# Kernel tuning notes

Measured on AMD Instinct MI355X. Metric: run time of the kernel, lower is better.

The kernel has to match this reference:

```python
import jax, jax.numpy as jnp
import numpy as np

N_NODES = 100000
N_EDGES = 1600000
IN_F = 64
OUT_F = 32
NEG_SLOPE = 0.2


def setup_inputs() -> dict:
    key = jax.random.key(0)
    k = jax.random.split(key, 6)
    x = jax.random.normal(k[0], (N_NODES, IN_F), dtype=jnp.float32)
    edge_index = jax.random.randint(k[1], (2, N_EDGES), 0, N_NODES, dtype=jnp.int64)
    W = jax.random.normal(k[2], (IN_F, OUT_F), dtype=jnp.float32) * 0.1
    att_src = jax.random.normal(k[3], (OUT_F,), dtype=jnp.float32) * 0.1
    att_dst = jax.random.normal(k[4], (OUT_F,), dtype=jnp.float32) * 0.1
    bias = jax.random.normal(k[5], (OUT_F,), dtype=jnp.float32) * 0.1
    return {"x": x, "edge_index": edge_index, "W": W,
            "att_src": att_src, "att_dst": att_dst, "bias": bias}


def reference(x, edge_index, W, att_src, att_dst, bias):
    N = x.shape[0]
    # Linear projection (single head, concat=True -> [N, OUT_F])
    h = x @ W  # [N, C]
    a_src = h @ att_src  # [N] per-node source attention logit contribution
    a_dst = h @ att_dst  # [N] per-node destination contribution
    # add self loops (PyG GATConv default add_self_loops=True)
    loop = jnp.arange(N, dtype=edge_index.dtype)
    src = jnp.concatenate([edge_index[0], loop])  # [E+N] message senders
    dst = jnp.concatenate([edge_index[1], loop])  # [E+N] message receivers
    # attention logits per edge, LeakyReLU(alpha_src[j] + alpha_dst[i])
    e = jax.nn.leaky_relu(a_src[src] + a_dst[dst], NEG_SLOPE)
    # segment softmax over incoming edges of each destination node
    m = jax.ops.segment_max(e, dst, num_segments=N)  # every node has a self loop
    ex = jnp.exp(e - m[dst])
    denom = jax.ops.segment_sum(ex, dst, num_segments=N)
    alpha = ex / denom[dst]  # [E+N]
    # weighted scatter-add of source features into destinations
    out = jax.ops.segment_sum(h[src] * alpha[:, None], dst, num_segments=N)
    out = out + bias
    # GATLayer activation='relu'
    return jax.nn.relu(out)
```

## Files before the change

kernel.cpp:

```cpp
#include <hip/hip_runtime.h>
#include <hip/hip_fp16.h>
#include <math.h>

#define IN_F 64
#define OUT_F 32
#define NEG_SLOPE 0.2f

#define BK_SHIFT 7
#define BK 128
#define NBMAX 1024
#define NBLKA 256
#define PSTAGE 10

typedef _Float16 half8_t __attribute__((ext_vector_type(8)));
typedef float float4_t __attribute__((ext_vector_type(4)));

__device__ __forceinline__ float leaky(float v) {
    return (v > 0.0f) ? v : NEG_SLOPE * v;
}

__device__ __forceinline__ int incScan256(int v, int tid, int* wsum) {
    const int lane = tid & 63, wid = tid >> 6;
    #pragma unroll
    for (int m = 1; m < 64; m <<= 1) {
        int u = __shfl_up(v, m);
        if (lane >= m) v += u;
    }
    if (lane == 63) wsum[wid] = v;
    __syncthreads();
    int add = 0;
    for (int k = 0; k < wid; ++k) add += wsum[k];
    __syncthreads();
    return v + add;
}

__device__ __forceinline__ int incScan512(int v, int tid, int* wsum) {
    const int lane = tid & 63, wid = tid >> 6;
    #pragma unroll
    for (int m = 1; m < 64; m <<= 1) {
        int u = __shfl_up(v, m);
        if (lane >= m) v += u;
    }
    if (lane == 63) wsum[wid] = v;
    __syncthreads();
    int add = 0;
    for (int k = 0; k < wid; ++k) add += wsum[k];
    __syncthreads();
    return v + add;
}

__global__ __launch_bounds__(256) void k_projhist(
        const float* __restrict__ x, const float* __restrict__ W,
        const float* __restrict__ att_src, const float* __restrict__ att_dst,
        __half2* __restrict__ h2, float* __restrict__ asrc, float* __restrict__ adst,
        const int* __restrict__ dst, int* __restrict__ hist,
        int N, int NB, int E, int epb, int PB) {
    __shared__ int smem[2560];
    const int tid = threadIdx.x;

    if (blockIdx.x >= PB) {
        int* lh = smem;
        const int blk = blockIdx.x - PB;
        for (int i = tid; i < NB; i += 256) lh[i] = 0;
        __syncthreads();
        const int e0 = blk * epb, e1 = min(E, e0 + epb);
        for (int e = e0 + tid; e < e1; e += 256) atomicAdd(&lh[dst[e] >> BK_SHIFT], 1);
        __syncthreads();
        for (int b = tid; b < NB; b += 256) hist[(size_t)b * NBLKA + blk] = lh[b];
        return;
    }

    const int wv   = tid >> 6;
    const int lane = tid & 63;
    const int m    = lane & 15;
    const int quad = lane >> 4;
    const int node0 = (blockIdx.x * 4 + wv) * 16;
    if (node0 >= N) return;

    const int kb = quad * 8;
    half8_t b00, b01, b10, b11;
    #pragma unroll
    for (int j = 0; j < 8; ++j) {
        b00[j] = (_Float16)W[(kb + j) * OUT_F + m];
        b01[j] = (_Float16)W[(32 + kb + j) * OUT_F + m];
        b10[j] = (_Float16)W[(kb + j) * OUT_F + 16 + m];
        b11[j] = (_Float16)W[(32 + kb + j) * OUT_F + 16 + m];
    }
    const int row = min(node0 + m, N - 1);
    const float* xr = x + (size_t)row * IN_F + kb;
    float4_t xa = *(const float4_t*)(xr);
    float4_t xb = *(const float4_t*)(xr + 4);
    float4_t xc = *(const float4_t*)(xr + 32);
    float4_t xd = *(const float4_t*)(xr + 36);
    half8_t a0, a1;
    #pragma unroll
    for (int j = 0; j < 4; ++j) {
        a0[j] = (_Float16)xa[j]; a0[4 + j] = (_Float16)xb[j];
        a1[j] = (_Float16)xc[j]; a1[4 + j] = (_Float16)xd[j];
    }
    float4_t acc0 = {0.f, 0.f, 0.f, 0.f};
    float4_t acc1 = {0.f, 0.f, 0.f, 0.f};
    acc0 = __builtin_amdgcn_mfma_f32_16x16x32_f16(a0, b00, acc0, 0, 0, 0);
    acc0 = __builtin_amdgcn_mfma_f32_16x16x32_f16(a1, b01, acc0, 0, 0, 0);
    acc1 = __builtin_amdgcn_mfma_f32_16x16x32_f16(a0, b10, acc1, 0, 0, 0);
    acc1 = __builtin_amdgcn_mfma_f32_16x16x32_f16(a1, b11, acc1, 0, 0, 0);

    const float aS0 = att_src[m], aS1 = att_src[16 + m];
    const float aD0 = att_dst[m], aD1 = att_dst[16 + m];
    #pragma unroll
    for (int r = 0; r < 4; ++r) {
        const int node = node0 + quad * 4 + r;
        float h0 = acc0[r], h1 = acc1[r];
        float h0p = __shfl_xor(h0, 1);
        float h1p = __shfl_xor(h1, 1);
        if (node < N && (m & 1) == 0) {
            __half2 hv;
            hv.x = __float2half_rn(h0); hv.y = __float2half_rn(h0p);
            h2[(size_t)node * 16 + (m >> 1)] = hv;
            __half2 hw;
            hw.x = __float2half_rn(h1); hw.y = __float2half_rn(h1p);
            h2[(size_t)node * 16 + 8 + (m >> 1)] = hw;
        }
        float vs = h0 * aS0 + h1 * aS1;
        float vd = h0 * aD0 + h1 * aD1;
        #pragma unroll
        for (int mm = 1; mm < 16; mm <<= 1) {
            vs += __shfl_xor(vs, mm);
            vd += __shfl_xor(vd, mm);
        }
        if (node < N && m == 0) {
            asrc[node] = vs;
            adst[node] = vd;
        }
    }
}

__global__ __launch_bounds__(256) void k_scan1(int* __restrict__ hist,
                                               int* __restrict__ bsum, int NB) {
    __shared__ int wsum[4];
    const int b = blockIdx.x, tid = threadIdx.x;
    int v = hist[(size_t)b * NBLKA + tid];
    const int inc = incScan256(v, tid, wsum);
    hist[(size_t)b * NBLKA + tid] = inc - v;
    if (tid == 255) bsum[b] = inc;
}

__global__ __launch_bounds__(512) void k_bpart(const int* __restrict__ src,
                                               const int* __restrict__ dst,
                                               const int* __restrict__ hist,
                                               const int* __restrict__ bsum,
                                               int* __restrict__ recs,
                                               int NB, int E, int epb) {
    __shared__ int tt[NBMAX];
    __shared__ int lcur[NBMAX];
    __shared__ int wsum[8];
    const int tid = threadIdx.x, blk = blockIdx.x;
    for (int i = tid; i < NBMAX; i += 512) tt[i] = (i < NB) ? bsum[i] : 0;
    __syncthreads();
    {
        int a0 = tt[tid * 2], a1 = tt[tid * 2 + 1];
        int s = a0 + a1;
        int inc = incScan512(s, tid, wsum);
        int run = inc - s;
        tt[tid * 2] = run; run += a0;
        tt[tid * 2 + 1] = run;
    }
    __syncthreads();
    for (int b = tid; b < NB; b += 512)
        lcur[b] = hist[(size_t)b * NBLKA + blk] + tt[b];
    __syncthreads();
    const int e0 = blk * epb, e1 = min(E, e0 + epb);
    for (int e = e0 + tid; e < e1; e += 512) {
        int s = src[e];
        int d = dst[e];
        int p = atomicAdd(&lcur[d >> BK_SHIFT], 1);
        recs[p] = ((d & (BK - 1)) << 17) | s;
    }
}

__global__ __launch_bounds__(256) void k_place(const int* __restrict__ recs,
                                               const int* __restrict__ bsum,
                                               int* __restrict__ cnt,
                                               int* __restrict__ offs,
                                               int* __restrict__ col,
                                               int NB, int E, int N) {
    __shared__ int tt[NBMAX];
    __shared__ int fineCnt[BK];
    __shared__ int cur[BK];
    __shared__ int wsum[4];
    const int b = blockIdx.x, tid = threadIdx.x;
    for (int i = tid; i < NBMAX; i += 256) tt[i] = (i < NB) ? bsum[i] : 0;
    __syncthreads();
    {
        int a0 = tt[tid * 4], a1 = tt[tid * 4 + 1], a2 = tt[tid * 4 + 2], a3 = tt[tid * 4 + 3];
        int s = a0 + a1 + a2 + a3;
        int inc = incScan256(s, tid, wsum);
        int run = inc - s;
        tt[tid * 4] = run;     run += a0;
        tt[tid * 4 + 1] = run; run += a1;
        tt[tid * 4 + 2] = run; run += a2;
        tt[tid * 4 + 3] = run;
    }
    __syncthreads();
    const int cb0 = tt[b];
    const int cb1 = (b + 1 < NB) ? tt[b + 1] : E;
    const int count = cb1 - cb0;
    int myrec[PSTAGE];
    if (tid < BK) fineCnt[tid] = 0;
    __syncthreads();
    #pragma unroll
    for (int k = 0; k < PSTAGE; ++k) {
        int i = tid + k * 256;
        if (i < count) {
            int v = recs[cb0 + i];
            myrec[k] = v;
            atomicAdd(&fineCnt[v >> 17], 1);
        }
    }
    for (int i = tid + PSTAGE * 256; i < count; i += 256)
        atomicAdd(&fineCnt[recs[cb0 + i] >> 17], 1);
    __syncthreads();
    const int v0 = (tid < BK) ? fineCnt[tid] : 0;
    const int inc = incScan256(v0, tid, wsum);
    const int excl = inc - v0;
    if (tid < BK) {
        const int node = (b << BK_SHIFT) + tid;
        if (node < N) {
            cnt[node]  = v0;
            offs[node] = cb0 + excl;
        }
        cur[tid] = cb0 + excl;
    }
    __syncthreads();
    #pragma unroll
    for (int k = 0; k < PSTAGE; ++k) {
        int i = tid + k * 256;
        if (i < count) {
            int r = myrec[k];
            int p = atomicAdd(&cur[r >> 17], 1);
            col[p] = r & 0x1FFFF;
        }
    }
    for (int i = tid + PSTAGE * 256; i < count; i += 256) {
        int r = recs[cb0 + i];
        int p = atomicAdd(&cur[r >> 17], 1);
        col[p] = r & 0x1FFFF;
    }
}

__global__ void k_gather(const int* __restrict__ col, const int* __restrict__ offs,
                         const int* __restrict__ cnt, const float* __restrict__ asrc,
                         const float* __restrict__ adst, const __half2* __restrict__ h2,
                         const float* __restrict__ bias, float* __restrict__ out, int N) {
    int t = blockIdx.x * 256 + threadIdx.x;
    int n = t >> 6;
    if (n >= N) return;
    const int lane = t & 63;
    const int g  = lane >> 4;
    const int c2 = lane & 15;
    const float adst_n = adst[n];
    float l = 0.0f, accx = 0.0f, accy = 0.0f;
    if (g == 0) {
        float p = __expf(leaky(asrc[n] + adst_n));
        float2 hv = __half22float2(h2[(size_t)n * 16 + c2]);
        l = p; accx = p * hv.x; accy = p * hv.y;
    }
    const int off = offs[n];
    const int deg = cnt[n];
    const int q = (deg + 3) >> 2;
    int j = off + g * q;
    const int jend = min(j + q, off + deg);
    for (; j < jend; j += 4) {
        const int last = jend - 1;
        int i1 = min(j + 1, last), i2 = min(j + 2, last), i3 = min(j + 3, last);
        int s0 = col[j], s1 = col[i1], s2 = col[i2], s3 = col[i3];
        float a0 = asrc[s0], a1 = asrc[s1], a2 = asrc[s2], a3 = asrc[s3];
        float2 h0 = __half22float2(h2[(size_t)s0 * 16 + c2]);
        float2 h1 = __half22float2(h2[(size_t)s1 * 16 + c2]);
        float2 hv2 = __half22float2(h2[(size_t)s2 * 16 + c2]);
        float2 h3 = __half22float2(h2[(size_t)s3 * 16 + c2]);
        float p0 = __expf(leaky(a0 + adst_n));
        float p1 = (j + 1 < jend) ? __expf(leaky(a1 + adst_n)) : 0.0f;
        float p2 = (j + 2 < jend) ? __expf(leaky(a2 + adst_n)) : 0.0f;
        float p3 = (j + 3 < jend) ? __expf(leaky(a3 + adst_n)) : 0.0f;
        l += (p0 + p1) + (p2 + p3);
        accx += p0 * h0.x + p1 * h1.x + p2 * hv2.x + p3 * h3.x;
        accy += p0 * h0.y + p1 * h1.y + p2 * hv2.y + p3 * h3.y;
    }
    l    += __shfl_xor(l, 16);    l    += __shfl_xor(l, 32);
    accx += __shfl_xor(accx, 16); accx += __shfl_xor(accx, 32);
    accy += __shfl_xor(accy, 16); accy += __shfl_xor(accy, 32);
    if (g == 0) {
        float inv = 1.0f / l;
        float2 bb = ((const float2*)bias)[c2];
        float2 o;
        o.x = fmaxf(accx * inv + bb.x, 0.0f);
        o.y = fmaxf(accy * inv + bb.y, 0.0f);
        ((float2*)out)[(size_t)n * 16 + c2] = o;
    }
}

extern "C" void kernel_launch(void* const* d_in, const int* in_sizes, int n_in,
                              void* d_out, int out_size, void* d_ws, size_t ws_size,
                              hipStream_t stream) {
    const float* x        = (const float*)d_in[0];
    const int*   eidx     = (const int*)d_in[1];
    const float* W        = (const float*)d_in[2];
    const float* att_src  = (const float*)d_in[3];
    const float* att_dst  = (const float*)d_in[4];
    const float* bias     = (const float*)d_in[5];
    float* out = (float*)d_out;

    const int N = in_sizes[0] / IN_F;
    const int E = in_sizes[1] / 2;
    const int* src = eidx;
    const int* dst = eidx + E;

    const int NB  = (N + BK - 1) >> BK_SHIFT;
    const int epb = (E + NBLKA - 1) / NBLKA;

    int* u = (int*)d_ws;
    size_t o = 0;
    __half2* h2   = (__half2*)(u + o); o += (size_t)N * 16;
    float*   asrc = (float*)(u + o);   o += N;
    float*   adst = (float*)(u + o);   o += N;
    int*     cnt  = u + o;             o += N;
    int*     offs = u + o;             o += N;
    int*     hist = u + o;             o += (size_t)NB * NBLKA;
    int*     bsum = u + o;             o += NBMAX;
    int*     col  = u + o;             o += E;
    int*     recs = u + o;             o += E;

    const int PB = (N + 63) / 64;
    const int gatherBlocks = ((size_t)N * 64 + 255) / 256;

    k_projhist<<<PB + NBLKA, 256, 0, stream>>>(x, W, att_src, att_dst, h2, asrc, adst,
                                               dst, hist, N, NB, E, epb, PB);
    k_scan1<<<NB, 256, 0, stream>>>(hist, bsum, NB);
    k_bpart<<<NBLKA, 512, 0, stream>>>(src, dst, hist, bsum, recs, NB, E, epb);
    k_place<<<NB, 256, 0, stream>>>(recs, bsum, cnt, offs, col, NB, E, N);
    k_gather<<<gatherBlocks, 256, 0, stream>>>(col, offs, cnt, asrc, adst, h2, bias, out, N);
}
```

Before: 169.3 us.

## Transpose bucket histogram layout and share edge logits via lane shuffles in gather

The per-block bucket histogram is stored block-major, so histogram writes and the partition kernel's reads become coalesced. The scan kernel now loads a 256x64 tile into LDS and runs a serial per-bucket scan across blocks, using fewer launched blocks. In the gather kernel, each of four lanes loads one column index and computes one exp logit, and the other lanes receive them by shuffle. This removes redundant asrc loads and exp calls at the cost of extra shuffles and a serial scan loop.

```diff
diff --git a/kernel.cpp b/kernel.cpp
--- a/kernel.cpp
+++ b/kernel.cpp
@@ -11,6 +11,7 @@
 #define NBMAX 1024
 #define NBLKA 256
 #define PSTAGE 10
+#define SB 64
 
 typedef _Float16 half8_t __attribute__((ext_vector_type(8)));
 typedef float float4_t __attribute__((ext_vector_type(4)));
@@ -66,7 +67,7 @@
         const int e0 = blk * epb, e1 = min(E, e0 + epb);
         for (int e = e0 + tid; e < e1; e += 256) atomicAdd(&lh[dst[e] >> BK_SHIFT], 1);
         __syncthreads();
-        for (int b = tid; b < NB; b += 256) hist[(size_t)b * NBLKA + blk] = lh[b];
+        for (int b = tid; b < NB; b += 256) hist[(size_t)blk * NB + b] = lh[b];
         return;
     }
 
@@ -137,12 +138,34 @@
 
 __global__ __launch_bounds__(256) void k_scan1(int* __restrict__ hist,
                                                int* __restrict__ bsum, int NB) {
-    __shared__ int wsum[4];
-    const int b = blockIdx.x, tid = threadIdx.x;
-    int v = hist[(size_t)b * NBLKA + tid];
-    const int inc = incScan256(v, tid, wsum);
-    hist[(size_t)b * NBLKA + tid] = inc - v;
-    if (tid == 255) bsum[b] = inc;
+    __shared__ int lbuf[NBLKA * SB];
+    const int bb0 = blockIdx.x * SB;
+    const int tid = threadIdx.x;
+    for (int i = tid; i < NBLKA * SB; i += 256) {
+        int blk = i >> 6;
+        int bo  = i & (SB - 1);
+        int b = bb0 + bo;
+        lbuf[blk * SB + bo] = (b < NB) ? hist[(size_t)blk * NB + b] : 0;
+    }
+    __syncthreads();
+    if (tid < SB) {
+        int run = 0;
+        #pragma unroll 8
+        for (int blk = 0; blk < NBLKA; ++blk) {
+            int v = lbuf[blk * SB + tid];
+            lbuf[blk * SB + tid] = run;
+            run += v;
+        }
+        int b = bb0 + tid;
+        if (b < NB) bsum[b] = run;
+    }
+    __syncthreads();
+    for (int i = tid; i < NBLKA * SB; i += 256) {
+        int blk = i >> 6;
+        int bo  = i & (SB - 1);
+        int b = bb0 + bo;
+        if (b < NB) hist[(size_t)blk * NB + b] = lbuf[blk * SB + bo];
+    }
 }
 
 __global__ __launch_bounds__(512) void k_bpart(const int* __restrict__ src,
@@ -167,7 +190,7 @@
     }
     __syncthreads();
     for (int b = tid; b < NB; b += 512)
-        lcur[b] = hist[(size_t)b * NBLKA + blk] + tt[b];
+        lcur[b] = hist[(size_t)blk * NB + b] + tt[b];
     __syncthreads();
     const int e0 = blk * epb, e1 = min(E, e0 + epb);
     for (int e = e0 + tid; e < e1; e += 512) {
@@ -258,6 +281,7 @@
     const int lane = t & 63;
     const int g  = lane >> 4;
     const int c2 = lane & 15;
+    const int eo = lane & 3;
     const float adst_n = adst[n];
     float l = 0.0f, accx = 0.0f, accy = 0.0f;
     if (g == 0) {
@@ -272,17 +296,20 @@
     const int jend = min(j + q, off + deg);
     for (; j < jend; j += 4) {
         const int last = jend - 1;
-        int i1 = min(j + 1, last), i2 = min(j + 2, last), i3 = min(j + 3, last);
-        int s0 = col[j], s1 = col[i1], s2 = col[i2], s3 = col[i3];
-        float a0 = asrc[s0], a1 = asrc[s1], a2 = asrc[s2], a3 = asrc[s3];
+        const int jo = j + eo;
+        int s0 = col[min(jo, last)];
+        float p0 = 0.0f;
+        if (jo <= last) p0 = __expf(leaky(asrc[s0] + adst_n));
+        int s1 = __shfl_xor(s0, 1);
+        int s2 = __shfl_xor(s0, 2);
+        int s3 = __shfl_xor(s0, 3);
+        float p1 = __shfl_xor(p0, 1);
+        float p2 = __shfl_xor(p0, 2);
+        float p3 = __shfl_xor(p0, 3);
         float2 h0 = __half22float2(h2[(size_t)s0 * 16 + c2]);
         float2 h1 = __half22float2(h2[(size_t)s1 * 16 + c2]);
         float2 hv2 = __half22float2(h2[(size_t)s2 * 16 + c2]);
         float2 h3 = __half22float2(h2[(size_t)s3 * 16 + c2]);
-        float p0 = __expf(leaky(a0 + adst_n));
-        float p1 = (j + 1 < jend) ? __expf(leaky(a1 + adst_n)) : 0.0f;
-        float p2 = (j + 2 < jend) ? __expf(leaky(a2 + adst_n)) : 0.0f;
-        float p3 = (j + 3 < jend) ? __expf(leaky(a3 + adst_n)) : 0.0f;
         l += (p0 + p1) + (p2 + p3);
         accx += p0 * h0.x + p1 * h1.x + p2 * hv2.x + p3 * h3.x;
         accy += p0 * h0.y + p1 * h1.y + p2 * hv2.y + p3 * h3.y;
@@ -326,17 +353,18 @@
     float*   adst = (float*)(u + o);   o += N;
     int*     cnt  = u + o;             o += N;
     int*     offs = u + o;             o += N;
-    int*     hist = u + o;             o += (size_t)NB * NBLKA;
+    int*     hist = u + o;             o += (size_t)NBLKA * NB;
     int*     bsum = u + o;             o += NBMAX;
     int*     col  = u + o;             o += E;
     int*     recs = u + o;             o += E;
 
     const int PB = (N + 63) / 64;
+    const int scanBlocks = (NB + SB - 1) / SB;
     const int gatherBlocks = ((size_t)N * 64 + 255) / 256;
 
     k_projhist<<<PB + NBLKA, 256, 0, stream>>>(x, W, att_src, att_dst, h2, asrc, adst,
                                                dst, hist, N, NB, E, epb, PB);
-    k_scan1<<<NB, 256, 0, stream>>>(hist, bsum, NB);
+    k_scan1<<<scanBlocks, 256, 0, stream>>>(hist, bsum, NB);
     k_bpart<<<NBLKA, 512, 0, stream>>>(src, dst, hist, bsum, recs, NB, E, epb);
     k_place<<<NB, 256, 0, stream>>>(recs, bsum, cnt, offs, col, NB, E, N);
     k_gather<<<gatherBlocks, 256, 0, stream>>>(col, offs, cnt, asrc, adst, h2, bias, out, N);
```

Result: slower. 194.7 us (+15.0%).

## Fuse fine CSR placement with per-destination gather into one block kernel

Applied to the files above, without the earlier changes.

Merges the k_place and k_gather kernels into a single k_bgather that sorts each 128-node bucket's edges into shared-memory columns and then performs the softmax-weighted aggregation directly from LDS. This removes the global col/offs/cnt arrays, one kernel launch, and a global round trip of the CSR column indices. Buckets with more than 4096 edges take a fallback path that accumulates with shared-memory float atomics instead. In exchange, the gather parallelism drops to one block per 128 nodes, about 782 blocks with 4 waves each looping over nodes. The larger shared footprint and PSTAGE raised to 16 may also lower occupancy.

```diff
diff --git a/kernel.cpp b/kernel.cpp
--- a/kernel.cpp
+++ b/kernel.cpp
@@ -10,7 +10,8 @@
 #define BK 128
 #define NBMAX 1024
 #define NBLKA 256
-#define PSTAGE 10
+#define LCAP 4096
+#define PSTAGE 16
 
 typedef _Float16 half8_t __attribute__((ext_vector_type(8)));
 typedef float float4_t __attribute__((ext_vector_type(4)));
@@ -178,17 +179,21 @@
     }
 }
 
-__global__ __launch_bounds__(256) void k_place(const int* __restrict__ recs,
-                                               const int* __restrict__ bsum,
-                                               int* __restrict__ cnt,
-                                               int* __restrict__ offs,
-                                               int* __restrict__ col,
-                                               int NB, int E, int N) {
-    __shared__ int tt[NBMAX];
-    __shared__ int fineCnt[BK];
-    __shared__ int cur[BK];
-    __shared__ int wsum[4];
+__global__ __launch_bounds__(256) void k_bgather(
+        const int* __restrict__ recs, const int* __restrict__ bsum,
+        const float* __restrict__ asrc, const float* __restrict__ adst,
+        const __half2* __restrict__ h2, const float* __restrict__ bias,
+        float* __restrict__ out, int NB, int E, int N) {
+    __shared__ int sh[5512];
+    int* tt      = sh;
+    int* lcol    = sh + 1024;
+    int* fineCnt = sh + 5120;
+    int* off2    = sh + 5248;
+    int* cur     = sh + 5376;
+    int* wsum    = sh + 5504;
     const int b = blockIdx.x, tid = threadIdx.x;
+    const int nb0 = b << BK_SHIFT;
+
     for (int i = tid; i < NBMAX; i += 256) tt[i] = (i < NB) ? bsum[i] : 0;
     __syncthreads();
     {
@@ -205,6 +210,46 @@
     const int cb0 = tt[b];
     const int cb1 = (b + 1 < NB) ? tt[b + 1] : E;
     const int count = cb1 - cb0;
+    __syncthreads();
+
+    if (count > LCAP) {
+        float* s_acc  = (float*)sh;
+        float* s_adst = (float*)(sh + 4224);
+        for (int i = tid; i < BK * 33; i += 256) s_acc[i] = 0.0f;
+        for (int i = tid; i < BK; i += 256) {
+            int n = nb0 + i;
+            s_adst[i] = (n < N) ? adst[n] : 0.0f;
+        }
+        __syncthreads();
+        const int slot = tid >> 4, c2 = tid & 15;
+        for (int i0 = 0; i0 < count; i0 += 16) {
+            int i = i0 + slot;
+            if (i < count) {
+                int r  = recs[cb0 + i];
+                int s  = r & 0x1FFFF;
+                int dl = r >> 17;
+                float p = __expf(leaky(asrc[s] + s_adst[dl]));
+                float2 hv = __half22float2(h2[(size_t)s * 16 + c2]);
+                atomicAdd(&s_acc[dl * 33 + 2 * c2],     p * hv.x);
+                atomicAdd(&s_acc[dl * 33 + 2 * c2 + 1], p * hv.y);
+                if (c2 == 0) atomicAdd(&s_acc[dl * 33 + 32], p);
+            }
+        }
+        __syncthreads();
+        const int c = tid & 31;
+        const float bc = bias[c];
+        for (int nl = tid >> 5; nl < BK; nl += 8) {
+            int n = nb0 + nl;
+            if (n >= N) break;
+            float pself = __expf(leaky(asrc[n] + s_adst[nl]));
+            float hc = __half2float(((const __half*)h2)[(size_t)n * 32 + c]);
+            float l = s_acc[nl * 33 + 32] + pself;
+            float v = (s_acc[nl * 33 + c] + pself * hc) / l + bc;
+            out[(size_t)n * 32 + c] = fmaxf(v, 0.0f);
+        }
+        return;
+    }
+
     int myrec[PSTAGE];
     if (tid < BK) fineCnt[tid] = 0;
     __syncthreads();
@@ -217,19 +262,14 @@
             atomicAdd(&fineCnt[v >> 17], 1);
         }
     }
-    for (int i = tid + PSTAGE * 256; i < count; i += 256)
-        atomicAdd(&fineCnt[recs[cb0 + i] >> 17], 1);
-    __syncthreads();
-    const int v0 = (tid < BK) ? fineCnt[tid] : 0;
-    const int inc = incScan256(v0, tid, wsum);
-    const int excl = inc - v0;
-    if (tid < BK) {
-        const int node = (b << BK_SHIFT) + tid;
-        if (node < N) {
-            cnt[node]  = v0;
-            offs[node] = cb0 + excl;
-        }
-        cur[tid] = cb0 + excl;
+    __syncthreads();
+    {
+        const int v0 = (tid < BK) ? fineCnt[tid] : 0;
+        const int inc = incScan256(v0, tid, wsum);
+        if (tid < BK) {
+            off2[tid] = inc - v0;
+            cur[tid]  = inc - v0;
+        }
     }
     __syncthreads();
     #pragma unroll
@@ -238,65 +278,57 @@
         if (i < count) {
             int r = myrec[k];
             int p = atomicAdd(&cur[r >> 17], 1);
-            col[p] = r & 0x1FFFF;
-        }
-    }
-    for (int i = tid + PSTAGE * 256; i < count; i += 256) {
-        int r = recs[cb0 + i];
-        int p = atomicAdd(&cur[r >> 17], 1);
-        col[p] = r & 0x1FFFF;
-    }
-}
-
-__global__ void k_gather(const int* __restrict__ col, const int* __restrict__ offs,
-                         const int* __restrict__ cnt, const float* __restrict__ asrc,
-                         const float* __restrict__ adst, const __half2* __restrict__ h2,
-                         const float* __restrict__ bias, float* __restrict__ out, int N) {
-    int t = blockIdx.x * 256 + threadIdx.x;
-    int n = t >> 6;
-    if (n >= N) return;
-    const int lane = t & 63;
+            lcol[p] = r & 0x1FFFF;
+        }
+    }
+    __syncthreads();
+
+    const int lane = tid & 63;
     const int g  = lane >> 4;
     const int c2 = lane & 15;
-    const float adst_n = adst[n];
-    float l = 0.0f, accx = 0.0f, accy = 0.0f;
-    if (g == 0) {
-        float p = __expf(leaky(asrc[n] + adst_n));
-        float2 hv = __half22float2(h2[(size_t)n * 16 + c2]);
-        l = p; accx = p * hv.x; accy = p * hv.y;
-    }
-    const int off = offs[n];
-    const int deg = cnt[n];
-    const int q = (deg + 3) >> 2;
-    int j = off + g * q;
-    const int jend = min(j + q, off + deg);
-    for (; j < jend; j += 4) {
-        const int last = jend - 1;
-        int i1 = min(j + 1, last), i2 = min(j + 2, last), i3 = min(j + 3, last);
-        int s0 = col[j], s1 = col[i1], s2 = col[i2], s3 = col[i3];
-        float a0 = asrc[s0], a1 = asrc[s1], a2 = asrc[s2], a3 = asrc[s3];
-        float2 h0 = __half22float2(h2[(size_t)s0 * 16 + c2]);
-        float2 h1 = __half22float2(h2[(size_t)s1 * 16 + c2]);
-        float2 hv2 = __half22float2(h2[(size_t)s2 * 16 + c2]);
-        float2 h3 = __half22float2(h2[(size_t)s3 * 16 + c2]);
-        float p0 = __expf(leaky(a0 + adst_n));
-        float p1 = (j + 1 < jend) ? __expf(leaky(a1 + adst_n)) : 0.0f;
-        float p2 = (j + 2 < jend) ? __expf(leaky(a2 + adst_n)) : 0.0f;
-        float p3 = (j + 3 < jend) ? __expf(leaky(a3 + adst_n)) : 0.0f;
-        l += (p0 + p1) + (p2 + p3);
-        accx += p0 * h0.x + p1 * h1.x + p2 * hv2.x + p3 * h3.x;
-        accy += p0 * h0.y + p1 * h1.y + p2 * hv2.y + p3 * h3.y;
-    }
-    l    += __shfl_xor(l, 16);    l    += __shfl_xor(l, 32);
-    accx += __shfl_xor(accx, 16); accx += __shfl_xor(accx, 32);
-    accy += __shfl_xor(accy, 16); accy += __shfl_xor(accy, 32);
-    if (g == 0) {
-        float inv = 1.0f / l;
-        float2 bb = ((const float2*)bias)[c2];
-        float2 o;
-        o.x = fmaxf(accx * inv + bb.x, 0.0f);
-        o.y = fmaxf(accy * inv + bb.y, 0.0f);
-        ((float2*)out)[(size_t)n * 16 + c2] = o;
+    for (int nl = tid >> 6; nl < BK; nl += 4) {
+        const int n = nb0 + nl;
+        if (n >= N) break;
+        const float adst_n = adst[n];
+        float l = 0.0f, accx = 0.0f, accy = 0.0f;
+        if (g == 0) {
+            float p = __expf(leaky(asrc[n] + adst_n));
+            float2 hv = __half22float2(h2[(size_t)n * 16 + c2]);
+            l = p; accx = p * hv.x; accy = p * hv.y;
+        }
+        const int off = off2[nl];
+        const int deg = fineCnt[nl];
+        const int q = (deg + 3) >> 2;
+        int j = off + g * q;
+        const int jend = min(j + q, off + deg);
+        for (; j < jend; j += 4) {
+            const int last = jend - 1;
+            int i1 = min(j + 1, last), i2 = min(j + 2, last), i3 = min(j + 3, last);
+            int s0 = lcol[j], s1 = lcol[i1], s2 = lcol[i2], s3 = lcol[i3];
+            float a0 = asrc[s0], a1 = asrc[s1], a2 = asrc[s2], a3 = asrc[s3];
+            float2 h0 = __half22float2(h2[(size_t)s0 * 16 + c2]);
+            float2 h1 = __half22float2(h2[(size_t)s1 * 16 + c2]);
+            float2 hv2 = __half22float2(h2[(size_t)s2 * 16 + c2]);
+            float2 h3 = __half22float2(h2[(size_t)s3 * 16 + c2]);
+            float p0 = __expf(leaky(a0 + adst_n));
+            float p1 = (j + 1 < jend) ? __expf(leaky(a1 + adst_n)) : 0.0f;
+            float p2 = (j + 2 < jend) ? __expf(leaky(a2 + adst_n)) : 0.0f;
+            float p3 = (j + 3 < jend) ? __expf(leaky(a3 + adst_n)) : 0.0f;
+            l += (p0 + p1) + (p2 + p3);
+            accx += p0 * h0.x + p1 * h1.x + p2 * hv2.x + p3 * h3.x;
+            accy += p0 * h0.y + p1 * h1.y + p2 * hv2.y + p3 * h3.y;
+        }
+        l    += __shfl_xor(l, 16);    l    += __shfl_xor(l, 32);
+        accx += __shfl_xor(accx, 16); accx += __shfl_xor(accx, 32);
+        accy += __shfl_xor(accy, 16); accy += __shfl_xor(accy, 32);
+        if (g == 0) {
+            float inv = 1.0f / l;
+            float2 bb = ((const float2*)bias)[c2];
+            float2 o;
+            o.x = fmaxf(accx * inv + bb.x, 0.0f);
+            o.y = fmaxf(accy * inv + bb.y, 0.0f);
+            ((float2*)out)[(size_t)n * 16 + c2] = o;
+        }
     }
 }
 
@@ -324,20 +356,15 @@
     __half2* h2   = (__half2*)(u + o); o += (size_t)N * 16;
     float*   asrc = (float*)(u + o);   o += N;
     float*   adst = (float*)(u + o);   o += N;
-    int*     cnt  = u + o;             o += N;
-    int*     offs = u + o;             o += N;
     int*     hist = u + o;             o += (size_t)NB * NBLKA;
     int*     bsum = u + o;             o += NBMAX;
-    int*     col  = u + o;             o += E;
     int*     recs = u + o;             o += E;
 
     const int PB = (N + 63) / 64;
-    const int gatherBlocks = ((size_t)N * 64 + 255) / 256;
 
     k_projhist<<<PB + NBLKA, 256, 0, stream>>>(x, W, att_src, att_dst, h2, asrc, adst,
                                                dst, hist, N, NB, E, epb, PB);
     k_scan1<<<NB, 256, 0, stream>>>(hist, bsum, NB);
     k_bpart<<<NBLKA, 512, 0, stream>>>(src, dst, hist, bsum, recs, NB, E, epb);
-    k_place<<<NB, 256, 0, stream>>>(recs, bsum, cnt, offs, col, NB, E, N);
-    k_gather<<<gatherBlocks, 256, 0, stream>>>(col, offs, cnt, asrc, adst, h2, bias, out, N);
-}
+    k_bgather<<<NB, 256, 0, stream>>>(recs, bsum, asrc, adst, h2, bias, out, NB, E, N);
+}
```

Measured after the change: 173.2 us. 1.02x slower.
